# Kernel optimization log

Measured on AMD Instinct MI355X. Metric: run time of the kernel, lower is better.

The kernel has to match this reference:

```python
import jax, jax.numpy as jnp
import numpy as np

B, C, H, W = 8, 256, 32, 32
N, COND_DIM, KV_DIM, REL_DIM = 512, 512, 512, 64
N_HEADS = 8
D_HEAD = KV_DIM // N_HEADS
K_SEL = int(N * 0.6)  # auto mode, shallow layer (layer_idx=2 < total_layers//2=4) -> centrality, ratio_shallow=0.6
NEG = -1e9


def _linear_params(key, fan_in, fan_out):
    kw, kb = jax.random.split(key)
    w = jax.random.normal(kw, (fan_out, fan_in), dtype=jnp.float32) / np.sqrt(fan_in)
    b = jax.random.normal(kb, (fan_out,), dtype=jnp.float32) * 0.01
    return w, b


def _normalize(x, axis=-1):
    # torch F.normalize: x / max(||x||_2, eps)
    n = jnp.sqrt(jnp.sum(x * x, axis=axis, keepdims=True))
    return x / jnp.maximum(n, 1e-12)


def setup_inputs() -> dict:
    key = jax.random.key(0)
    ks = jax.random.split(key, 10)
    h = jax.random.normal(ks[0], (B, C, H, W), dtype=jnp.float32)
    cond_feats = jax.random.normal(ks[1], (B, N, COND_DIM), dtype=jnp.float32)
    cond_mask = jax.random.randint(ks[2], (B, N), 0, 2) > 0  # bool, 1 valid
    Wq, bq = _linear_params(ks[3], C, KV_DIM)
    Wk, bk = _linear_params(ks[4], COND_DIM, KV_DIM)
    Wv, bv = _linear_params(ks[5], COND_DIM, KV_DIM)
    Wrq, brq = _linear_params(ks[6], C, REL_DIM)
    Wrk, brk = _linear_params(ks[7], COND_DIM, REL_DIM)
    Wo, bo = _linear_params(ks[8], KV_DIM, C)
    return dict(h=h, cond_feats=cond_feats, cond_mask=cond_mask,
                Wq=Wq, bq=bq, Wk=Wk, bk=bk, Wv=Wv, bv=bv,
                Wrq=Wrq, brq=brq, Wrk=Wrk, brk=brk, Wo=Wo, bo=bo)


def reference(h, cond_feats, cond_mask, Wq, bq, Wk, bk, Wv, bv, Wrq, brq, Wrk, brk, Wo, bo):
    Bq, Ch, Hh, Ww = h.shape
    S = Hh * Ww
    # ---- q/k/v projections ----
    q = h.reshape(Bq, Ch, S).transpose(0, 2, 1)                # (B,S,C)
    q = q @ Wq.T + bq                                           # (B,S,KV)
    K = cond_feats @ Wk.T + bk                                  # (B,N,KV)
    V = cond_feats @ Wv.T + bv
    qh = q.reshape(Bq, S, N_HEADS, D_HEAD).transpose(0, 2, 1, 3)
    kh = K.reshape(Bq, N, N_HEADS, D_HEAD).transpose(0, 2, 1, 3)
    vh = V.reshape(Bq, N, N_HEADS, D_HEAD).transpose(0, 2, 1, 3)
    attn_scores = jnp.einsum('bhqd,bhkd->bhqk', qh, kh) / np.sqrt(D_HEAD)
    # ---- selector: auto mode, shallow -> centrality scores ----
    qg = h.mean(axis=(2, 3))                                    # adaptive_avg_pool2d(h,1) -> (B,C)
    qg_proj = _normalize(qg @ Wrq.T + brq)                      # (B,REL)  (unused branch kept faithful)
    cond_proj = _normalize(cond_feats @ Wrk.T + brk)            # (B,N,REL)
    Smat = jnp.einsum('bnd,bmd->bnm', cond_proj, cond_proj)     # (B,N,N)
    eye = jnp.eye(N, dtype=bool)
    centrality = jnp.where(eye[None], 0.0, Smat).sum(axis=-1)   # (B,N)
    scores = centrality
    # ---- top-k mask via scatter ----
    topk_idx = jax.lax.top_k(scores, K_SEL)[1]                  # (B,K)
    selected = jnp.zeros((Bq, N), dtype=bool).at[jnp.arange(Bq)[:, None], topk_idx].set(True)
    allowed = selected & cond_mask
    rows_all_false = ~allowed.any(axis=1)                       # (B,)
    idx0 = jnp.argmax(scores, axis=-1)                          # top-1 fallback
    fallback = jax.nn.one_hot(idx0, N, dtype=bool)
    allowed = allowed | (rows_all_false[:, None] & fallback)
    attn_scores = jnp.where(allowed[:, None, None, :], attn_scores, NEG)
    # ---- attention ----
    attn = jax.nn.softmax(attn_scores, axis=-1)
    out = jnp.einsum('bhqk,bhkd->bhqd', attn, vh)               # (B,h,S,d)
    out = out.transpose(0, 2, 1, 3).reshape(Bq, S, KV_DIM)
    out = out @ Wo.T + bo                                       # (B,S,C)
    return out.transpose(0, 2, 1).reshape(Bq, Ch, Hh, Ww)
```

## Files before the change

kernel.cpp:

```cpp
#include <hip/hip_runtime.h>
#include <math.h>

#define B_ 8
#define C_ 256
#define S_ 1024
#define N_ 512
#define KV_ 512
#define REL_ 64
#define NH_ 8
#define DH_ 64
#define KSEL_ 307

#define BM 128
#define BN 128

typedef __attribute__((ext_vector_type(8))) short bf16x8;
typedef __attribute__((ext_vector_type(4))) short short4v;
typedef __attribute__((ext_vector_type(4))) float f32x4;

__device__ __forceinline__ short f2bf(float f) {
  unsigned int u = __float_as_uint(f);
  u += 0x7fffu + ((u >> 16) & 1u);
  return (short)(u >> 16);
}

__global__ __launch_bounds__(256) void k_prep(const float* __restrict__ cond, const float* __restrict__ Wq,
                                              const float* __restrict__ Wk, const float* __restrict__ Wv,
                                              const float* __restrict__ Wo, const float* __restrict__ h,
                                              const float* __restrict__ Wrk,
                                              short* __restrict__ cond_b, short* __restrict__ Wq_b,
                                              short* __restrict__ Wk_b, short* __restrict__ Wv_b,
                                              short* __restrict__ Wo_b, short* __restrict__ hT,
                                              float* __restrict__ cp_part) {
  __shared__ float fs[2176];
  int blk = blockIdx.x, tid = threadIdx.x;
  if (blk < 2816) {
    const float* src; short* dst; int base;
    if (blk < 2048)      { src = cond; dst = cond_b; base = blk; }
    else if (blk < 2176) { src = Wq;   dst = Wq_b;   base = blk - 2048; }
    else if (blk < 2432) { src = Wk;   dst = Wk_b;   base = blk - 2176; }
    else if (blk < 2688) { src = Wv;   dst = Wv_b;   base = blk - 2432; }
    else                 { src = Wo;   dst = Wo_b;   base = blk - 2688; }
    int i = base * 256 + tid;
    float4 v = ((const float4*)src)[i];
    short4v o = { f2bf(v.x), f2bf(v.y), f2bf(v.z), f2bf(v.w) };
    ((short4v*)dst)[i] = o;
  } else if (blk < 4864) {
    int i = blk - 2816;
    int s0 = (i & 31) * 32, c0 = ((i >> 5) & 7) * 32, b = i >> 8;
    int x = tid & 31, y0 = tid >> 5;
    #pragma unroll
    for (int y = y0; y < 32; y += 8)
      fs[y * 33 + x] = h[((size_t)(b * C_ + c0 + y)) * S_ + s0 + x];
    __syncthreads();
    #pragma unroll
    for (int y = y0; y < 32; y += 8)
      hT[((size_t)(b * S_ + s0 + y)) * C_ + c0 + x] = f2bf(fs[x * 33 + y]);
  } else {
    int i = blk - 4864;
    int bm = (i & 63) * 64, kb = i >> 6;
    float* As = fs;
    float* Bs = fs + 1088;
    int tm = (tid >> 4) << 2, tn = (tid & 15) << 2;
    float acc[4][4] = {};
    for (int k0 = kb * 128; k0 < kb * 128 + 128; k0 += 16) {
      #pragma unroll
      for (int ii = 0; ii < 4; ++ii) {
        int idx = tid + ii * 256;
        int r = idx >> 4, k = idx & 15;
        As[r * 17 + k] = cond[(size_t)(bm + r) * KV_ + k0 + k];
        Bs[r * 17 + k] = Wrk[(size_t)r * KV_ + k0 + k];
      }
      __syncthreads();
      #pragma unroll
      for (int k = 0; k < 16; ++k) {
        float a[4], bb[4];
        #pragma unroll
        for (int x = 0; x < 4; ++x) { a[x] = As[(tm + x) * 17 + k]; bb[x] = Bs[(tn + x) * 17 + k]; }
        #pragma unroll
        for (int x = 0; x < 4; ++x)
          #pragma unroll
          for (int y = 0; y < 4; ++y)
            acc[x][y] += a[x] * bb[y];
      }
      __syncthreads();
    }
    #pragma unroll
    for (int x = 0; x < 4; ++x)
      #pragma unroll
      for (int y = 0; y < 4; ++y)
        cp_part[(size_t)kb * 262144 + (size_t)(bm + tm + x) * 64 + tn + y] = acc[x][y];
  }
}

__global__ __launch_bounds__(256) void k_normalize(const float* __restrict__ cp_part, const float* __restrict__ brk,
                                                   float* __restrict__ cp) {
  int row = blockIdx.x * 4 + (threadIdx.x >> 6);
  int d = threadIdx.x & 63;
  size_t off = (size_t)row * 64 + d;
  float x = cp_part[off] + cp_part[262144 + off] + cp_part[524288 + off] + cp_part[786432 + off] + brk[d];
  float ss = x * x;
  #pragma unroll
  for (int o = 32; o; o >>= 1) ss += __shfl_xor(ss, o);
  cp[off] = x / fmaxf(sqrtf(ss), 1e-12f);
}

__global__ __launch_bounds__(512) void k_select(const float* __restrict__ cp, const int* __restrict__ mask,
                                                int* __restrict__ idxb, int* __restrict__ cnt) {
  int b = blockIdx.x, tid = threadIdx.x;
  __shared__ float part[8][64];
  __shared__ float vsum[64];
  __shared__ float sc[512];
  __shared__ int wcnt[8];
  int d = tid & 63, g = tid >> 6;
  float sacc = 0.f;
  for (int n = g * 64; n < g * 64 + 64; ++n)
    sacc += cp[((size_t)b * N_ + n) * 64 + d];
  part[g][d] = sacc;
  __syncthreads();
  if (tid < 64) {
    float v = 0.f;
    #pragma unroll
    for (int gg = 0; gg < 8; ++gg) v += part[gg][tid];
    vsum[tid] = v;
  }
  __syncthreads();
  const float* x = cp + ((size_t)b * N_ + tid) * 64;
  float dsum = 0.f, dself = 0.f;
  #pragma unroll
  for (int dd = 0; dd < 64; ++dd) {
    float xv = x[dd];
    dsum += xv * vsum[dd];
    dself += xv * xv;
  }
  sc[tid] = dsum - dself;
  __syncthreads();
  float v = sc[tid];
  int rank = 0;
  for (int j = 0; j < N_; ++j) {
    float u = sc[j];
    rank += (u > v) || (u == v && j < tid);
  }
  int sel = (rank < KSEL_) && (mask[b * N_ + tid] != 0);
  unsigned long long bal = __ballot(sel);
  if ((tid & 63) == 0) wcnt[g] = __popcll(bal);
  __syncthreads();
  int off2 = 0, total = 0;
  #pragma unroll
  for (int i = 0; i < 8; ++i) { int c = wcnt[i]; total += c; if (i < g) off2 += c; }
  int pos = off2 + __popcll(bal & ((1ull << (tid & 63)) - 1ull));
  if (sel) idxb[b * N_ + pos] = tid;
  if (total == 0 && rank == 0) idxb[b * N_] = tid;
  if (tid == 0) cnt[b] = (total == 0) ? 1 : total;
}

template<int MODE, int GA, int GB>
__device__ __forceinline__ void gemm_body(const short* __restrict__ A, const short* __restrict__ W,
                                          const float* __restrict__ bias, void* __restrict__ Cout,
                                          short* As, short* Bs, size_t bm, size_t bn, int Kd, int Nout,
                                          const int* __restrict__ gidx, int cntv) {
  int tid = threadIdx.x;
  int lane = tid & 63, wid = tid >> 6;
  int wr = wid >> 1, wc = wid & 1;
  f32x4 acc[4][4] = {};
  int srow = lane >> 2;
  int schunk = lane & 3;
  int steps = Kd >> 5;

  int rowA[2], rowB[2];
  #pragma unroll
  for (int i = 0; i < 2; ++i) {
    int rt = wid * 32 + i * 16 + srow;
    rowA[i] = GA ? (((int)bm + rt < cntv) ? gidx[bm + rt] : 0) : (int)(bm + rt);
    rowB[i] = GB ? (((int)bn + rt < cntv) ? gidx[bn + rt] : 0) : (int)(bn + rt);
  }

  #define STAGE_G(t, buf)                                                                              \
    {                                                                                                  \
      int k0s = (t) * 32;                                                                              \
      _Pragma("unroll")                                                                                \
      for (int i = 0; i < 2; ++i) {                                                                    \
        int rt = wid * 32 + i * 16 + srow;                                                             \
        int sc_ = (schunk ^ ((rt >> 1) & 3)) * 8;                                                      \
        const short* ga = A + (size_t)rowA[i] * Kd + k0s + sc_;                                        \
        __builtin_amdgcn_global_load_lds((const __attribute__((address_space(1))) void*)ga,            \
            (__attribute__((address_space(3))) void*)(As + (buf) * 4096 + (wid * 32 + i * 16) * 32),   \
            16, 0, 0);                                                                                 \
        const short* gb = W + (size_t)rowB[i] * Kd + k0s + sc_;                                        \
        __builtin_amdgcn_global_load_lds((const __attribute__((address_space(1))) void*)gb,            \
            (__attribute__((address_space(3))) void*)(Bs + (buf) * 4096 + (wid * 32 + i * 16) * 32),   \
            16, 0, 0);                                                                                 \
      }                                                                                                \
    }

  STAGE_G(0, 0);
  asm volatile("s_waitcnt vmcnt(0)" ::: "memory");
  __syncthreads();

  for (int t = 0; t < steps; ++t) {
    int cur = t & 1;
    if (t + 1 < steps) STAGE_G(t + 1, cur ^ 1);
    const short* Ac = As + cur * 4096;
    const short* Bc = Bs + cur * 4096;
    bf16x8 a[4], b[4];
    #pragma unroll
    for (int m = 0; m < 4; ++m) {
      int rt = wr * 64 + m * 16 + (lane & 15);
      a[m] = *(const bf16x8*)(Ac + rt * 32 + (((lane >> 4) ^ ((rt >> 1) & 3)) * 8));
    }
    #pragma unroll
    for (int n = 0; n < 4; ++n) {
      int rt = wc * 64 + n * 16 + (lane & 15);
      b[n] = *(const bf16x8*)(Bc + rt * 32 + (((lane >> 4) ^ ((rt >> 1) & 3)) * 8));
    }
    __builtin_amdgcn_s_setprio(1);
    #pragma unroll
    for (int m = 0; m < 4; ++m)
      #pragma unroll
      for (int n = 0; n < 4; ++n)
        acc[m][n] = __builtin_amdgcn_mfma_f32_16x16x32_bf16(a[m], b[n], acc[m][n], 0, 0, 0);
    __builtin_amdgcn_s_setprio(0);
    asm volatile("s_waitcnt vmcnt(0)" ::: "memory");
    __syncthreads();
  }
  #undef STAGE_G

  int c0 = lane & 15, r0q = lane >> 4;
  #pragma unroll
  for (int n = 0; n < 4; ++n) {
    size_t col = bn + wc * 64 + n * 16 + c0;
    #pragma unroll
    for (int m = 0; m < 4; ++m) {
      #pragma unroll
      for (int j = 0; j < 4; ++j) {
        size_t row = bm + wr * 64 + m * 16 + r0q * 4 + j;
        if (MODE == 0) {
          ((short*)Cout)[row * Nout + col] = f2bf(acc[m][n][j] + bias[col]);
        } else if (MODE == 1) {
          ((float*)Cout)[((col >> 10) * C_ + row) * S_ + (col & (S_ - 1))] = acc[m][n][j] + bias[row];
        } else {
          ((short*)Cout)[row * Nout + col] = f2bf(acc[m][n][j] + bias[row]);
        }
      }
    }
  }
}

__global__ __launch_bounds__(256) void k_fused_proj(const short* __restrict__ hT, const short* __restrict__ cond_b,
                                                    const short* __restrict__ Wq_b, const short* __restrict__ Wk_b,
                                                    const short* __restrict__ Wv_b,
                                                    const float* __restrict__ bq, const float* __restrict__ bk,
                                                    const float* __restrict__ bv,
                                                    short* __restrict__ qb, short* __restrict__ Kc,
                                                    short* __restrict__ Vtc,
                                                    const int* __restrict__ idxb, const int* __restrict__ cnt) {
  __shared__ short smem[16384];
  int blk = blockIdx.x;
  if (blk < 256) {
    gemm_body<0, 0, 0>(hT, Wq_b, bq, qb, smem, smem + 8192,
                       (size_t)(blk & 63) * 128, (size_t)(blk >> 6) * 128, C_, KV_, nullptr, 0);
  } else if (blk < 352) {
    int i = blk - 256, b = i / 12, j = i % 12;
    int mt = j >> 2, ntile = j & 3;
    int cv = cnt[b], padded = (cv + 63) & ~63;
    if (mt * 128 >= padded) return;
    gemm_body<0, 1, 0>(cond_b + (size_t)b * N_ * KV_, Wk_b, bk, Kc + (size_t)b * N_ * KV_,
                       smem, smem + 8192, (size_t)mt * 128, (size_t)ntile * 128, KV_, KV_,
                       idxb + b * N_, cv);
  } else {
    int i = blk - 352, b = i / 12, j = i % 12;
    int mtd = j & 3, ntc = j >> 2;
    int cv = cnt[b], padded = (cv + 63) & ~63;
    if (ntc * 128 >= padded) return;
    gemm_body<3, 0, 1>(Wv_b, cond_b + (size_t)b * N_ * KV_, bv, Vtc + (size_t)b * 512 * N_,
                       smem, smem + 8192, (size_t)mtd * 128, (size_t)ntc * 128, KV_, N_,
                       idxb + b * N_, cv);
  }
}

__device__ __forceinline__ void stage_tile64(const short* gRowBase, int gStride, short* ldsBase, int wid, int lane) {
  int sub = lane >> 3;
  int colE = ((lane & 7) ^ sub) * 8;
  #pragma unroll
  for (int i = 0; i < 2; ++i) {
    int r = wid * 16 + i * 8 + sub;
    const short* gp = gRowBase + (size_t)r * gStride + colE;
    __builtin_amdgcn_global_load_lds((const __attribute__((address_space(1))) void*)gp,
                                     (__attribute__((address_space(3))) void*)(ldsBase + wid * 1024 + i * 512),
                                     16, 0, 0);
  }
}
__device__ __forceinline__ void stage_tile64_w8(const short* gRowBase, int gStride, short* ldsBase, int wid, int lane) {
  int sub = lane >> 3;
  int colE = ((lane & 7) ^ sub) * 8;
  int r = wid * 8 + sub;
  const short* gp = gRowBase + (size_t)r * gStride + colE;
  __builtin_amdgcn_global_load_lds((const __attribute__((address_space(1))) void*)gp,
                                   (__attribute__((address_space(3))) void*)(ldsBase + wid * 512),
                                   16, 0, 0);
}

#define QK2L 0.18033688f
__global__ __launch_bounds__(512) void k_attn_mfma(const short* __restrict__ qb, const short* __restrict__ Kc,
                                                   const short* __restrict__ Vtc, const int* __restrict__ cnt,
                                                   short* __restrict__ attn_b) {
  __shared__ short Qs[8192];
  __shared__ short Ks[2][4096];
  __shared__ short Vs[2][4096];
  __shared__ short Ps[8192];
  int g = blockIdx.x;
  int xcd = g & 7, li = g >> 3;
  int bh = xcd * 8 + (li >> 3);
  int qt = li & 7;
  int b = bh >> 3, h = bh & 7;
  int tid = threadIdx.x, lane = tid & 63, wid = tid >> 6;
  int hi = lane >> 4, q = lane & 15;
  int s0 = qt * 128;
  int cntv = cnt[b];
  int nt = (cntv + 63) >> 6;
  const short* Qg = qb + ((size_t)(b * S_ + s0) * KV_ + h * DH_);
  const short* Kg = Kc + ((size_t)(b * N_) * KV_ + h * DH_);
  const short* Vg = Vtc + ((size_t)((b * NH_ + h) * DH_) * N_);

  stage_tile64(Qg, KV_, Qs, wid, lane);
  stage_tile64_w8(Kg, KV_, Ks[0], wid, lane);
  stage_tile64_w8(Vg, N_, Vs[0], wid, lane);
  asm volatile("s_waitcnt vmcnt(0)" ::: "memory");
  __syncthreads();

  int swz = (lane & 7) << 3;
  bf16x8 qf0 = *(const bf16x8*)&Qs[(wid * 16 + q) * 64 + ((hi * 8) ^ swz)];
  bf16x8 qf1 = *(const bf16x8*)&Qs[(wid * 16 + q) * 64 + ((32 + hi * 8) ^ swz)];

  float m = -1e30f, l = 0.f;
  f32x4 o[4] = {};

  for (int t = 0; t < nt; ++t) {
    int cur = t & 1;
    const short* Kcur = Ks[cur];
    const short* Vcur = Vs[cur];
    if (t + 1 < nt) {
      stage_tile64_w8(Kg + (size_t)(t + 1) * 64 * KV_, KV_, Ks[cur ^ 1], wid, lane);
      stage_tile64_w8(Vg + (t + 1) * 64, N_, Vs[cur ^ 1], wid, lane);
    }
    f32x4 pv[4];
    __builtin_amdgcn_s_setprio(1);
    #pragma unroll
    for (int kf = 0; kf < 4; ++kf) {
      bf16x8 k0 = *(const bf16x8*)&Kcur[(kf * 16 + q) * 64 + ((hi * 8) ^ swz)];
      bf16x8 k1 = *(const bf16x8*)&Kcur[(kf * 16 + q) * 64 + ((32 + hi * 8) ^ swz)];
      f32x4 z = {0.f, 0.f, 0.f, 0.f};
      pv[kf] = __builtin_amdgcn_mfma_f32_16x16x32_bf16(k0, qf0, z, 0, 0, 0);
      pv[kf] = __builtin_amdgcn_mfma_f32_16x16x32_bf16(k1, qf1, pv[kf], 0, 0, 0);
    }
    __builtin_amdgcn_s_setprio(0);
    float sv[16];
    int kbase = t * 64 + hi * 4;
    #pragma unroll
    for (int kf = 0; kf < 4; ++kf) {
      #pragma unroll
      for (int r = 0; r < 4; ++r)
        sv[kf * 4 + r] = (kbase + kf * 16 + r < cntv) ? pv[kf][r] * QK2L : -1e30f;
    }
    float tmax = sv[0];
    #pragma unroll
    for (int i = 1; i < 16; ++i) tmax = fmaxf(tmax, sv[i]);
    tmax = fmaxf(tmax, __shfl_xor(tmax, 16));
    tmax = fmaxf(tmax, __shfl_xor(tmax, 32));
    float mnew = fmaxf(m, tmax);
    float scale = exp2f(m - mnew);
    float psum = 0.f;
    #pragma unroll
    for (int i = 0; i < 16; ++i) { sv[i] = exp2f(sv[i] - mnew); psum += sv[i]; }
    psum += __shfl_xor(psum, 16);
    psum += __shfl_xor(psum, 32);
    l = l * scale + psum;
    m = mnew;
    #pragma unroll
    for (int df = 0; df < 4; ++df) {
      o[df][0] *= scale; o[df][1] *= scale; o[df][2] *= scale; o[df][3] *= scale;
    }
    int pbase = wid * 1024 + q * 64;
    #pragma unroll
    for (int kf = 0; kf < 4; ++kf) {
      short4v pk = { f2bf(sv[kf * 4 + 0]), f2bf(sv[kf * 4 + 1]), f2bf(sv[kf * 4 + 2]), f2bf(sv[kf * 4 + 3]) };
      *(short4v*)&Ps[pbase + ((kf * 16 + hi * 4) ^ swz)] = pk;
    }
    __builtin_amdgcn_s_setprio(1);
    #pragma unroll
    for (int ks = 0; ks < 2; ++ks) {
      bf16x8 pb = *(const bf16x8*)&Ps[pbase + ((ks * 32 + hi * 8) ^ swz)];
      #pragma unroll
      for (int df = 0; df < 4; ++df) {
        bf16x8 vf = *(const bf16x8*)&Vcur[(df * 16 + q) * 64 + ((ks * 32 + hi * 8) ^ swz)];
        o[df] = __builtin_amdgcn_mfma_f32_16x16x32_bf16(vf, pb, o[df], 0, 0, 0);
      }
    }
    __builtin_amdgcn_s_setprio(0);
    asm volatile("s_waitcnt vmcnt(0)" ::: "memory");
    __syncthreads();
  }
  float inv = 1.0f / l;
  short* op = attn_b + ((size_t)(b * S_ + s0 + wid * 16 + q) * KV_ + h * DH_);
  #pragma unroll
  for (int df = 0; df < 4; ++df) {
    short4v ov = { f2bf(o[df][0] * inv), f2bf(o[df][1] * inv), f2bf(o[df][2] * inv), f2bf(o[df][3] * inv) };
    *(short4v*)&op[df * 16 + hi * 4] = ov;
  }
}

__global__ __launch_bounds__(256) void k_outproj(const short* __restrict__ Wo_b, const short* __restrict__ attn_b,
                                                 const float* __restrict__ bo, float* __restrict__ out) {
  __shared__ short smem[16384];
  gemm_body<1, 0, 0>(Wo_b, attn_b, bo, out, smem, smem + 8192,
                     (size_t)blockIdx.x * 128, (size_t)blockIdx.y * 128, KV_, B_ * S_, nullptr, 0);
}

extern "C" void kernel_launch(void* const* d_in, const int* in_sizes, int n_in,
                              void* d_out, int out_size, void* d_ws, size_t ws_size,
                              hipStream_t stream) {
  const float* h         = (const float*)d_in[0];
  const float* cond      = (const float*)d_in[1];
  const int*   cond_mask = (const int*)d_in[2];
  const float* Wq = (const float*)d_in[3];
  const float* bq = (const float*)d_in[4];
  const float* Wk = (const float*)d_in[5];
  const float* bk = (const float*)d_in[6];
  const float* Wv = (const float*)d_in[7];
  const float* bv = (const float*)d_in[8];
  const float* Wrk = (const float*)d_in[11];
  const float* brk = (const float*)d_in[12];
  const float* Wo  = (const float*)d_in[13];
  const float* bo  = (const float*)d_in[14];
  float* out = (float*)d_out;

  char* w = (char*)d_ws;
  short* qb      = (short*)(w + 0);
  short* Kc      = (short*)(w + 8388608);
  short* Vtc     = (short*)(w + 12582912);
  short* attn_b  = (short*)(w + 16777216);
  short* hT      = (short*)(w + 25165824);
  short* cond_b  = (short*)(w + 29360128);
  float* cp_part = (float*)(w + 33554432);
  float* cp      = (float*)(w + 37748736);
  int*   idxb    = (int*)  (w + 38797312);
  int*   cnt     = (int*)  (w + 38813696);
  short* Wq_b    = (short*)(w + 38813760);
  short* Wk_b    = (short*)(w + 39075904);
  short* Wv_b    = (short*)(w + 39600192);
  short* Wo_b    = (short*)(w + 40124480);

  k_prep<<<5120, 256, 0, stream>>>(cond, Wq, Wk, Wv, Wo, h, Wrk,
                                   cond_b, Wq_b, Wk_b, Wv_b, Wo_b, hT, cp_part);
  k_normalize<<<1024, 256, 0, stream>>>(cp_part, brk, cp);
  k_select<<<8, 512, 0, stream>>>(cp, cond_mask, idxb, cnt);
  k_fused_proj<<<448, 256, 0, stream>>>(hT, cond_b, Wq_b, Wk_b, Wv_b, bq, bk, bv,
                                        qb, Kc, Vtc, idxb, cnt);
  k_attn_mfma<<<512, 512, 0, stream>>>(qb, Kc, Vtc, cnt, attn_b);
  k_outproj<<<dim3(2, 64), 256, 0, stream>>>(Wo_b, attn_b, bo, out);
}
```

Measured before the change: 106.5 us.

## Increase parallelism: finer split-K for cond projection, smaller outproj tiles, reorder proj blocks

Splits the cond·Wrk split-K reduction into 8 chunks of 64 instead of 4 of 128, giving twice as many prep blocks, and sums 8 partials in normalize. Templatizes the GEMM body on the M tile so the output projection uses 64-row tiles and launches twice as many blocks to fill more CUs. Reorders fused projection blocks so the variable-size K/V gathers are scheduled before the Q projection. Costs are more partial-sum traffic and less per-block reuse in the out projection.

Measured after the change: 99.18 us. 6.8% less time.

```diff
diff --git a/kernel.cpp b/kernel.cpp
--- a/kernel.cpp
+++ b/kernel.cpp
@@ -10,9 +10,6 @@
 #define NH_ 8
 #define DH_ 64
 #define KSEL_ 307
-
-#define BM 128
-#define BN 128
 
 typedef __attribute__((ext_vector_type(8))) short bf16x8;
 typedef __attribute__((ext_vector_type(4))) short short4v;
@@ -63,7 +60,7 @@
     float* Bs = fs + 1088;
     int tm = (tid >> 4) << 2, tn = (tid & 15) << 2;
     float acc[4][4] = {};
-    for (int k0 = kb * 128; k0 < kb * 128 + 128; k0 += 16) {
+    for (int k0 = kb * 64; k0 < kb * 64 + 64; k0 += 16) {
       #pragma unroll
       for (int ii = 0; ii < 4; ++ii) {
         int idx = tid + ii * 256;
@@ -98,7 +95,9 @@
   int row = blockIdx.x * 4 + (threadIdx.x >> 6);
   int d = threadIdx.x & 63;
   size_t off = (size_t)row * 64 + d;
-  float x = cp_part[off] + cp_part[262144 + off] + cp_part[524288 + off] + cp_part[786432 + off] + brk[d];
+  float x = brk[d];
+  #pragma unroll
+  for (int s = 0; s < 8; ++s) x += cp_part[(size_t)s * 262144 + off];
   float ss = x * x;
   #pragma unroll
   for (int o = 32; o; o >>= 1) ss += __shfl_xor(ss, o);
@@ -154,24 +153,30 @@
   if (tid == 0) cnt[b] = (total == 0) ? 1 : total;
 }
 
-template<int MODE, int GA, int GB>
+template<int MODE, int GA, int GB, int WM>
 __device__ __forceinline__ void gemm_body(const short* __restrict__ A, const short* __restrict__ W,
                                           const float* __restrict__ bias, void* __restrict__ Cout,
                                           short* As, short* Bs, size_t bm, size_t bn, int Kd, int Nout,
                                           const int* __restrict__ gidx, int cntv) {
+  constexpr int BMv = WM * 32;
+  constexpr int NIA = BMv / 64;
   int tid = threadIdx.x;
   int lane = tid & 63, wid = tid >> 6;
   int wr = wid >> 1, wc = wid & 1;
-  f32x4 acc[4][4] = {};
+  f32x4 acc[WM][4] = {};
   int srow = lane >> 2;
   int schunk = lane & 3;
   int steps = Kd >> 5;
 
-  int rowA[2], rowB[2];
+  int rowA[NIA], rowB[2];
+  #pragma unroll
+  for (int i = 0; i < NIA; ++i) {
+    int rt = wid * (WM * 8) + i * 16 + srow;
+    rowA[i] = GA ? (((int)bm + rt < cntv) ? gidx[bm + rt] : 0) : (int)(bm + rt);
+  }
   #pragma unroll
   for (int i = 0; i < 2; ++i) {
     int rt = wid * 32 + i * 16 + srow;
-    rowA[i] = GA ? (((int)bm + rt < cntv) ? gidx[bm + rt] : 0) : (int)(bm + rt);
     rowB[i] = GB ? (((int)bn + rt < cntv) ? gidx[bn + rt] : 0) : (int)(bn + rt);
   }
 
@@ -179,13 +184,19 @@
     {                                                                                                  \
       int k0s = (t) * 32;                                                                              \
       _Pragma("unroll")                                                                                \
+      for (int i = 0; i < NIA; ++i) {                                                                  \
+        int rt = wid * (WM * 8) + i * 16 + srow;                                                       \
+        int sc_ = (schunk ^ ((rt >> 1) & 3)) * 8;                                                      \
+        const short* ga = A + (size_t)rowA[i] * Kd + k0s + sc_;                                        \
+        __builtin_amdgcn_global_load_lds((const __attribute__((address_space(1))) void*)ga,            \
+            (__attribute__((address_space(3))) void*)(As + (buf) * (BMv * 32) +                        \
+                                                     (wid * (WM * 8) + i * 16) * 32),                  \
+            16, 0, 0);                                                                                 \
+      }                                                                                                \
+      _Pragma("unroll")                                                                                \
       for (int i = 0; i < 2; ++i) {                                                                    \
         int rt = wid * 32 + i * 16 + srow;                                                             \
         int sc_ = (schunk ^ ((rt >> 1) & 3)) * 8;                                                      \
-        const short* ga = A + (size_t)rowA[i] * Kd + k0s + sc_;                                        \
-        __builtin_amdgcn_global_load_lds((const __attribute__((address_space(1))) void*)ga,            \
-            (__attribute__((address_space(3))) void*)(As + (buf) * 4096 + (wid * 32 + i * 16) * 32),   \
-            16, 0, 0);                                                                                 \
         const short* gb = W + (size_t)rowB[i] * Kd + k0s + sc_;                                        \
         __builtin_amdgcn_global_load_lds((const __attribute__((address_space(1))) void*)gb,            \
             (__attribute__((address_space(3))) void*)(Bs + (buf) * 4096 + (wid * 32 + i * 16) * 32),   \
@@ -200,12 +211,12 @@
   for (int t = 0; t < steps; ++t) {
     int cur = t & 1;
     if (t + 1 < steps) STAGE_G(t + 1, cur ^ 1);
-    const short* Ac = As + cur * 4096;
+    const short* Ac = As + cur * (BMv * 32);
     const short* Bc = Bs + cur * 4096;
-    bf16x8 a[4], b[4];
-    #pragma unroll
-    for (int m = 0; m < 4; ++m) {
-      int rt = wr * 64 + m * 16 + (lane & 15);
+    bf16x8 a[WM], b[4];
+    #pragma unroll
+    for (int m = 0; m < WM; ++m) {
+      int rt = wr * (WM * 16) + m * 16 + (lane & 15);
       a[m] = *(const bf16x8*)(Ac + rt * 32 + (((lane >> 4) ^ ((rt >> 1) & 3)) * 8));
     }
     #pragma unroll
@@ -215,7 +226,7 @@
     }
     __builtin_amdgcn_s_setprio(1);
     #pragma unroll
-    for (int m = 0; m < 4; ++m)
+    for (int m = 0; m < WM; ++m)
       #pragma unroll
       for (int n = 0; n < 4; ++n)
         acc[m][n] = __builtin_amdgcn_mfma_f32_16x16x32_bf16(a[m], b[n], acc[m][n], 0, 0, 0);
@@ -230,10 +241,10 @@
   for (int n = 0; n < 4; ++n) {
     size_t col = bn + wc * 64 + n * 16 + c0;
     #pragma unroll
-    for (int m = 0; m < 4; ++m) {
+    for (int m = 0; m < WM; ++m) {
       #pragma unroll
       for (int j = 0; j < 4; ++j) {
-        size_t row = bm + wr * 64 + m * 16 + r0q * 4 + j;
+        size_t row = bm + wr * (WM * 16) + m * 16 + r0q * 4 + j;
         if (MODE == 0) {
           ((short*)Cout)[row * Nout + col] = f2bf(acc[m][n][j] + bias[col]);
         } else if (MODE == 1) {
@@ -256,25 +267,26 @@
                                                     const int* __restrict__ idxb, const int* __restrict__ cnt) {
   __shared__ short smem[16384];
   int blk = blockIdx.x;
-  if (blk < 256) {
-    gemm_body<0, 0, 0>(hT, Wq_b, bq, qb, smem, smem + 8192,
-                       (size_t)(blk & 63) * 128, (size_t)(blk >> 6) * 128, C_, KV_, nullptr, 0);
-  } else if (blk < 352) {
-    int i = blk - 256, b = i / 12, j = i % 12;
+  if (blk < 96) {
+    int b = blk / 12, j = blk % 12;
     int mt = j >> 2, ntile = j & 3;
     int cv = cnt[b], padded = (cv + 63) & ~63;
     if (mt * 128 >= padded) return;
-    gemm_body<0, 1, 0>(cond_b + (size_t)b * N_ * KV_, Wk_b, bk, Kc + (size_t)b * N_ * KV_,
-                       smem, smem + 8192, (size_t)mt * 128, (size_t)ntile * 128, KV_, KV_,
-                       idxb + b * N_, cv);
-  } else {
-    int i = blk - 352, b = i / 12, j = i % 12;
+    gemm_body<0, 1, 0, 4>(cond_b + (size_t)b * N_ * KV_, Wk_b, bk, Kc + (size_t)b * N_ * KV_,
+                          smem, smem + 8192, (size_t)mt * 128, (size_t)ntile * 128, KV_, KV_,
+                          idxb + b * N_, cv);
+  } else if (blk < 192) {
+    int i = blk - 96, b = i / 12, j = i % 12;
     int mtd = j & 3, ntc = j >> 2;
     int cv = cnt[b], padded = (cv + 63) & ~63;
     if (ntc * 128 >= padded) return;
-    gemm_body<3, 0, 1>(Wv_b, cond_b + (size_t)b * N_ * KV_, bv, Vtc + (size_t)b * 512 * N_,
-                       smem, smem + 8192, (size_t)mtd * 128, (size_t)ntc * 128, KV_, N_,
-                       idxb + b * N_, cv);
+    gemm_body<3, 0, 1, 4>(Wv_b, cond_b + (size_t)b * N_ * KV_, bv, Vtc + (size_t)b * 512 * N_,
+                          smem, smem + 8192, (size_t)mtd * 128, (size_t)ntc * 128, KV_, N_,
+                          idxb + b * N_, cv);
+  } else {
+    int i = blk - 192;
+    gemm_body<0, 0, 0, 4>(hT, Wq_b, bq, qb, smem, smem + 8192,
+                          (size_t)(i & 63) * 128, (size_t)(i >> 6) * 128, C_, KV_, nullptr, 0);
   }
 }
 
@@ -411,9 +423,9 @@
 
 __global__ __launch_bounds__(256) void k_outproj(const short* __restrict__ Wo_b, const short* __restrict__ attn_b,
                                                  const float* __restrict__ bo, float* __restrict__ out) {
-  __shared__ short smem[16384];
-  gemm_body<1, 0, 0>(Wo_b, attn_b, bo, out, smem, smem + 8192,
-                     (size_t)blockIdx.x * 128, (size_t)blockIdx.y * 128, KV_, B_ * S_, nullptr, 0);
+  __shared__ short smem[12288];
+  gemm_body<1, 0, 0, 2>(Wo_b, attn_b, bo, out, smem, smem + 4096,
+                        (size_t)blockIdx.x * 64, (size_t)blockIdx.y * 128, KV_, B_ * S_, nullptr, 0);
 }
 
 extern "C" void kernel_launch(void* const* d_in, const int* in_sizes, int n_in,
@@ -442,20 +454,20 @@
   short* hT      = (short*)(w + 25165824);
   short* cond_b  = (short*)(w + 29360128);
   float* cp_part = (float*)(w + 33554432);
-  float* cp      = (float*)(w + 37748736);
-  int*   idxb    = (int*)  (w + 38797312);
-  int*   cnt     = (int*)  (w + 38813696);
-  short* Wq_b    = (short*)(w + 38813760);
-  short* Wk_b    = (short*)(w + 39075904);
-  short* Wv_b    = (short*)(w + 39600192);
-  short* Wo_b    = (short*)(w + 40124480);
-
-  k_prep<<<5120, 256, 0, stream>>>(cond, Wq, Wk, Wv, Wo, h, Wrk,
+  float* cp      = (float*)(w + 41943040);
+  int*   idxb    = (int*)  (w + 42991616);
+  int*   cnt     = (int*)  (w + 43008000);
+  short* Wq_b    = (short*)(w + 43008064);
+  short* Wk_b    = (short*)(w + 43270208);
+  short* Wv_b    = (short*)(w + 43794496);
+  short* Wo_b    = (short*)(w + 44318784);
+
+  k_prep<<<5376, 256, 0, stream>>>(cond, Wq, Wk, Wv, Wo, h, Wrk,
                                    cond_b, Wq_b, Wk_b, Wv_b, Wo_b, hT, cp_part);
   k_normalize<<<1024, 256, 0, stream>>>(cp_part, brk, cp);
   k_select<<<8, 512, 0, stream>>>(cp, cond_mask, idxb, cnt);
   k_fused_proj<<<448, 256, 0, stream>>>(hT, cond_b, Wq_b, Wk_b, Wv_b, bq, bk, bv,
                                         qb, Kc, Vtc, idxb, cnt);
   k_attn_mfma<<<512, 512, 0, stream>>>(qb, Kc, Vtc, cnt, attn_b);
-  k_outproj<<<dim3(2, 64), 256, 0, stream>>>(Wo_b, attn_b, bo, out);
-}
+  k_outproj<<<dim3(4, 64), 256, 0, stream>>>(Wo_b, attn_b, bo, out);
+}
```
